# Optimization experiments

Measured on AMD Instinct MI355X. Metric: run time of the kernel, lower is better.

## Reference

```python
import jax, jax.numpy as jnp
import numpy as np
import math

B, S, K, D, H, LH, W, L = 8, 2048, 128, 512, 8, 4, 128, 4
DH = D // H           # 64, head dim
NW = S // W           # 16 windows
NUM_STEPS = 1000
RESCALE = 4000.0


def setup_inputs() -> dict:
    key = jax.random.key(0)
    ks = iter(jax.random.split(key, 48))
    def rn(shape, s=0.02):
        return jax.random.normal(next(ks), shape, dtype=jnp.float32) * s
    return {
        "x": jax.random.normal(next(ks), (B, S, K), dtype=jnp.float32),
        "t": jax.random.randint(next(ks), (B,), 0, NUM_STEPS, dtype=jnp.int32),
        "token_w": rn((K, D)), "token_b": jnp.zeros((D,), jnp.float32),
        "ax1": rn((NW, D), 1.0), "ax2": rn((W, D), 1.0),
        "time_w1": rn((D, 4 * D)), "time_b1": jnp.zeros((4 * D,), jnp.float32),
        "time_w2": rn((4 * D, D)), "time_b2": jnp.zeros((D,), jnp.float32),
        "ln1_g": jnp.ones((L, D), jnp.float32), "ln1_b": jnp.zeros((L, D), jnp.float32),
        "wq": rn((L, D, D)), "wk": rn((L, D, D)), "wv": rn((L, D, D)),
        "wo": rn((L, D, D)), "wo_b": jnp.zeros((L, D), jnp.float32),
        "ln2_g": jnp.ones((L, D), jnp.float32), "ln2_b": jnp.zeros((L, D), jnp.float32),
        "ff_w1": rn((L, D, 4 * D)), "ff_b1": jnp.zeros((L, 4 * D), jnp.float32),
        "ff_w2": rn((L, 4 * D, D)), "ff_b2": jnp.zeros((L, D), jnp.float32),
        "norm_g": jnp.ones((D,), jnp.float32), "norm_b": jnp.zeros((D,), jnp.float32),
        "out_w": rn((D, K)), "out_b": jnp.zeros((K,), jnp.float32),
        "alpha": jax.random.normal(next(ks), (1,), dtype=jnp.float32),
    }


def _layernorm(x, g, b, eps=1e-5):
    mu = x.mean(-1, keepdims=True)
    var = ((x - mu) ** 2).mean(-1, keepdims=True)
    return (x - mu) * jax.lax.rsqrt(var + eps) * g + b


def _mish(x):
    return x * jnp.tanh(jax.nn.softplus(x))


def _sinusoidal(t):
    # SinusoidalPosEmb(dim=D, num_steps=NUM_STEPS, rescale_steps=4000)
    tt = t.astype(jnp.float32) / NUM_STEPS * RESCALE
    half = D // 2
    freqs = jnp.exp(jnp.arange(half, dtype=jnp.float32) * (-math.log(10000.0) / (half - 1)))
    e = tt[:, None] * freqs[None, :]
    return jnp.concatenate([jnp.sin(e), jnp.cos(e)], axis=-1)  # (B, D)


def _linear_attn(q, k, v):
    # non-causal kernelized linear attention; q,k,v: (B, h, S, dh)
    scale = DH ** -0.25
    q = jax.nn.softmax(q * scale, axis=-1)   # softmax over feature dim
    k = jax.nn.softmax(k * scale, axis=-2)   # softmax over sequence dim
    ctx = jnp.einsum('bhnd,bhne->bhde', k, v)
    return jnp.einsum('bhnd,bhde->bhne', q, ctx)


def _local_attn(q, k, v):
    # windowed softmax attention, window W, look_backward=1, look_forward=1
    b, h = q.shape[0], q.shape[1]
    qw = q.reshape(b, h, NW, W, DH) * (DH ** -0.5)
    def look_around(x):
        xw = x.reshape(b, h, NW, W, DH)
        xp = jnp.pad(xw, ((0, 0), (0, 0), (1, 1), (0, 0), (0, 0)))
        # keys of windows [i-1, i, i+1] -> (b, h, NW, 3W, dh)
        return jnp.concatenate([xp[:, :, :-2], xp[:, :, 1:-1], xp[:, :, 2:]], axis=3)
    kw, vw = look_around(k), look_around(v)
    win = jnp.arange(NW)[:, None] + (jnp.arange(3 * W) // W)[None, :] - 1  # (NW, 3W)
    valid = (win >= 0) & (win < NW)
    dots = jnp.einsum('bhnwd,bhnkd->bhnwk', qw, kw)
    mask_value = -jnp.finfo(dots.dtype).max
    dots = jnp.where(valid[None, None, :, None, :], dots, mask_value)
    attn = jax.nn.softmax(dots, axis=-1)
    out = jnp.einsum('bhnwk,bhnkd->bhnwd', attn, vw)
    return out.reshape(b, h, S, DH)


def reference(x, t, token_w, token_b, ax1, ax2, time_w1, time_b1, time_w2, time_b2,
              ln1_g, ln1_b, wq, wk, wv, wo, wo_b, ln2_g, ln2_b,
              ff_w1, ff_b1, ff_w2, ff_b2, norm_g, norm_b, out_w, out_b, alpha):
    te = _sinusoidal(t)
    te = _mish(te @ time_w1 + time_b1) @ time_w2 + time_b2          # (B, D)
    h = x @ token_w + token_b                                        # token embedding
    pos = (ax1[:, None, :] + ax2[None, :, :]).reshape(S, D)          # axial pos emb (summed)
    h = h + pos[None] + te[:, None, :]
    for l in range(L):
        n = _layernorm(h, ln1_g[l], ln1_b[l])
        def split_heads(y):
            return y.reshape(B, S, H, DH).transpose(0, 2, 1, 3)
        q = split_heads(n @ wq[l]); k = split_heads(n @ wk[l]); v = split_heads(n @ wv[l])
        lo = _local_attn(q[:, :LH], k[:, :LH], v[:, :LH])            # local heads first
        gl = _linear_attn(q[:, LH:], k[:, LH:], v[:, LH:])           # global linear-attn heads
        a = jnp.concatenate([lo, gl], axis=1).transpose(0, 2, 1, 3).reshape(B, S, D)
        h = h + a @ wo[l] + wo_b[l]
        n = _layernorm(h, ln2_g[l], ln2_b[l])
        h = h + jax.nn.gelu(n @ ff_w1[l] + ff_b1[l], approximate=False) @ ff_w2[l] + ff_b2[l]
    out = _layernorm(h, norm_g, norm_b) @ out_w + out_b              # (B, S, K)
    return alpha * out.transpose(0, 2, 1)                            # permute + Rezero -> (B, K, S)
```

## Files before the change

### kernel.cpp

```cpp
#include <hip/hip_runtime.h>

typedef __bf16 bf16;
typedef float f32x4 __attribute__((ext_vector_type(4)));
typedef __bf16 b8v __attribute__((ext_vector_type(8)));
typedef __bf16 b4v __attribute__((ext_vector_type(4)));

#define S_LEN 2048
#define DMODEL 512
#define KDIM 128
#define NWIN 16
#define WIN 128
#define QKVS 1536

__device__ inline f32x4 mfma16(b8v a, b8v b, f32x4 c) {
  return __builtin_amdgcn_mfma_f32_16x16x32_bf16(a, b, c, 0, 0, 0);
}

__device__ inline void gload16(const bf16* g, bf16* l) {
  __builtin_amdgcn_global_load_lds(
      (const __attribute__((address_space(1))) void*)g,
      (__attribute__((address_space(3))) void*)l, 16, 0, 0);
}

template<int N>
__device__ inline void waitvm() { asm volatile("s_waitcnt vmcnt(%0)" :: "n"(N) : "memory"); }
template<int N>
__device__ inline void waitlgkm() { asm volatile("s_waitcnt lgkmcnt(%0)" :: "n"(N) : "memory"); }
__device__ inline void barrier_raw() { asm volatile("s_barrier" ::: "memory"); }


__global__ __launch_bounds__(256) void conv_kernel(const float* __restrict__ in, bf16* __restrict__ out, int n) {
  int i4 = (blockIdx.x * 256 + threadIdx.x) * 4;
  if (i4 < n) {
    float4 v = *(const float4*)(in + i4);
    b4v o; o[0] = (bf16)v.x; o[1] = (bf16)v.y; o[2] = (bf16)v.z; o[3] = (bf16)v.w;
    *(b4v*)(out + i4) = o;
  }
}

__global__ __launch_bounds__(256) void convT_kernel(const float* __restrict__ W, bf16* __restrict__ WT,
                                                    int Kd, int N, size_t in_ls, size_t out_ls) {
  __shared__ float tile[32][33];
  int k0 = blockIdx.x * 32, n0 = blockIdx.y * 32;
  const float* Wl = W + (size_t)blockIdx.z * in_ls;
  bf16* WTl = WT + (size_t)blockIdx.z * out_ls;
  int tx = threadIdx.x & 31, ty = threadIdx.x >> 5;
  #pragma unroll
  for (int i = 0; i < 4; i++)
    tile[ty + i*8][tx] = Wl[(size_t)(k0 + ty + i*8) * N + n0 + tx];
  __syncthreads();
  #pragma unroll
  for (int i = 0; i < 4; i++)
    WTl[(size_t)(n0 + ty + i*8) * Kd + k0 + tx] = (bf16)tile[tx][ty + i*8];
}

__global__ __launch_bounds__(256) void convT4_kernel(
    const float* __restrict__ wq, const float* __restrict__ wk,
    const float* __restrict__ wv, const float* __restrict__ wo,
    bf16* __restrict__ wqkvT, bf16* __restrict__ woT) {
  __shared__ float tile[32][33];
  int z = blockIdx.z, layer = z >> 2, which = z & 3;
  const float* W = (which == 0 ? wq : which == 1 ? wk : which == 2 ? wv : wo)
                   + (size_t)layer * 262144;
  bf16* WT = (which < 3) ? (wqkvT + (size_t)layer * 786432 + (size_t)which * 262144)
                         : (woT + (size_t)layer * 262144);
  int k0 = blockIdx.x * 32, n0 = blockIdx.y * 32;
  int tx = threadIdx.x & 31, ty = threadIdx.x >> 5;
  #pragma unroll
  for (int i = 0; i < 4; i++)
    tile[ty + i*8][tx] = W[(size_t)(k0 + ty + i*8) * 512 + n0 + tx];
  __syncthreads();
  #pragma unroll
  for (int i = 0; i < 4; i++)
    WT[(size_t)(n0 + ty + i*8) * 512 + k0 + tx] = (bf16)tile[tx][ty + i*8];
}


__global__ __launch_bounds__(256) void time1_kernel(const int* __restrict__ t,
    const float* __restrict__ w1, const float* __restrict__ b1, float* __restrict__ te1) {
  __shared__ float te[512];
  __shared__ float red[4][64];
  int b = blockIdx.x >> 5;
  int c0 = (blockIdx.x & 31) * 64;
  int tid = threadIdx.x;
  float tt = (float)t[b] * 4.0f;
  {
    float fr = expf((float)tid * (-9.210340371976184f / 255.0f));
    float e = tt * fr;
    te[tid] = sinf(e);
    te[tid + 256] = cosf(e);
  }
  __syncthreads();
  int lane = tid & 63, wv = tid >> 6;
  float acc = 0.f;
  const float* wcol = w1 + (size_t)(wv * 128) * 2048 + c0 + lane;
  for (int dd = 0; dd < 128; dd++) acc = fmaf(te[wv * 128 + dd], wcol[(size_t)dd * 2048], acc);
  red[wv][lane] = acc;
  __syncthreads();
  if (tid < 64) {
    float a = red[0][tid] + red[1][tid] + red[2][tid] + red[3][tid] + b1[c0 + tid];
    float sp = (a > 20.f) ? a : log1pf(expf(a));
    te1[b * 2048 + c0 + tid] = a * tanhf(sp);
  }
}

__global__ __launch_bounds__(256) void time2_kernel(const float* __restrict__ te1,
    const float* __restrict__ w2, const float* __restrict__ b2, float* __restrict__ te2) {
  __shared__ float hb[2048];
  __shared__ float red[4][64];
  int b = blockIdx.x >> 3;
  int c0 = (blockIdx.x & 7) * 64;
  int tid = threadIdx.x;
  for (int i = tid; i < 2048; i += 256) hb[i] = te1[b * 2048 + i];
  __syncthreads();
  int lane = tid & 63, wv = tid >> 6;
  float acc = 0.f;
  const float* wcol = w2 + (size_t)(wv * 512) * 512 + c0 + lane;
  for (int dd = 0; dd < 512; dd++) acc = fmaf(hb[wv * 512 + dd], wcol[(size_t)dd * 512], acc);
  red[wv][lane] = acc;
  __syncthreads();
  if (tid < 64)
    te2[b * 512 + c0 + tid] = red[0][tid] + red[1][tid] + red[2][tid] + red[3][tid] + b2[c0 + tid];
}


__global__ __launch_bounds__(256) void ln_kernel(const bf16* __restrict__ hsrc,
    const float* __restrict__ gg, const float* __restrict__ bb, bf16* __restrict__ out) {
  int row = blockIdx.x * 4 + (threadIdx.x >> 6);
  int lane = threadIdx.x & 63;
  const bf16* hr = hsrc + (size_t)row * 512 + lane * 8;
  b8v hv = *(const b8v*)hr;
  float xv[8];
  #pragma unroll
  for (int j = 0; j < 8; j++) xv[j] = (float)hv[j];
  float s = 0.f;
  #pragma unroll
  for (int j = 0; j < 8; j++) s += xv[j];
  #pragma unroll
  for (int off = 1; off < 64; off <<= 1) s += __shfl_xor(s, off);
  float mu = s * (1.f / 512.f);
  float vs = 0.f;
  #pragma unroll
  for (int j = 0; j < 8; j++) { float dd = xv[j] - mu; vs += dd * dd; }
  #pragma unroll
  for (int off = 1; off < 64; off <<= 1) vs += __shfl_xor(vs, off);
  float rstd = 1.f / sqrtf(vs * (1.f / 512.f) + 1e-5f);
  int dbase = lane * 8;
  bf16* orow = out + (size_t)row * 512 + dbase;
  #pragma unroll
  for (int j = 0; j < 8; j++)
    orow[j] = (bf16)((xv[j] - mu) * rstd * gg[dbase + j] + bb[dbase + j]);
}

template<int EPI, int BM, int BN>
__global__ __launch_bounds__(512, 2) void gemm3_kernel(
    const bf16* __restrict__ A, const bf16* __restrict__ BT,
    const float* __restrict__ bias, bf16* __restrict__ Cb,
    int N, int Kd, int nbx) {
  constexpr int LA = BM / 128;
  constexpr int LB = BN / 128;
  constexpr int LPI = LA + LB;
  constexpr int EA = BM * 32;
  constexpr int EB = BN * 32;
  constexpr int ER = EA + EB;
  constexpr int MF = BM / 32;
  constexpr int NF = BN / 64;
  __shared__ bf16 lds[ER * 3];
  int tid = threadIdx.x;
  int lane = tid & 63, wid = tid >> 6;
  int g = lane >> 4, lr = lane & 15;
  int wm = wid >> 2, wn = wid & 3;
  int p = blockIdx.x;
  int cpx = (int)gridDim.x >> 3;
  int vid = (p & 7) * cpx + (p >> 3);
  int m0 = (vid / nbx) * BM;
  int n0 = (vid % nbx) * BN;
  f32x4 acc[MF][NF] = {};
  int rl = tid >> 2;
  int csw = ((tid & 3) ^ ((rl >> 1) & 3)) * 8;
  const bf16* pa = A + (size_t)(m0 + rl) * Kd + csw;
  const bf16* pb = BT + (size_t)(n0 + rl) * Kd + csw;
  int NT = Kd >> 5;
  auto stage = [&](int t, int buf) {
    int k0 = t << 5;
    bf16* base = lds + buf * ER + (wid << 9);
    #pragma unroll
    for (int rr = 0; rr < LA; rr++)
      gload16(pa + (size_t)(rr * 128) * Kd + k0, base + rr * 4096);
    #pragma unroll
    for (int rr = 0; rr < LB; rr++)
      gload16(pb + (size_t)(rr * 128) * Kd + k0, base + EA + rr * 4096);
  };
  stage(0, 0);
  stage(1, 1);
  for (int kt = 0; kt < NT; ++kt) {
    if (kt + 1 < NT) waitvm<LPI>();
    else             waitvm<0>();
    barrier_raw();
    const bf16* ba = lds + (kt % 3) * ER;
    const bf16* bb = ba + EA;
    if (kt + 2 < NT) stage(kt + 2, (kt + 2) % 3);
    b8v af[MF], bfr[NF];
    #pragma unroll
    for (int i = 0; i < MF; i++) {
      int ra = wm * (BM / 2) + i * 16 + lr;
      af[i] = *(const b8v*)(ba + ra * 32 + ((g * 8) ^ (((ra >> 1) & 3) << 3)));
    }
    #pragma unroll
    for (int j0 = 0; j0 < 2; j0++) {
      int rb = wn * (BN / 4) + j0 * 16 + lr;
      bfr[j0] = *(const b8v*)(bb + rb * 32 + ((g * 8) ^ (((rb >> 1) & 3) << 3)));
    }
    waitlgkm<0>();
    __builtin_amdgcn_sched_barrier(0);
    __builtin_amdgcn_s_setprio(1);
    #pragma unroll
    for (int i = 0; i < MF; i++) acc[i][0] = mfma16(af[i], bfr[0], acc[i][0]);
    __builtin_amdgcn_s_setprio(0);
    #pragma unroll
    for (int j = 1; j < NF; j++) {
      if (j + 1 < NF) {
        int rb = wn * (BN / 4) + (j + 1) * 16 + lr;
        bfr[j + 1] = *(const b8v*)(bb + rb * 32 + ((g * 8) ^ (((rb >> 1) & 3) << 3)));
        waitlgkm<1>();
      } else {
        waitlgkm<0>();
      }
      __builtin_amdgcn_sched_barrier(0);
      __builtin_amdgcn_s_setprio(1);
      #pragma unroll
      for (int i = 0; i < MF; i++) acc[i][j] = mfma16(af[i], bfr[j], acc[i][j]);
      __builtin_amdgcn_s_setprio(0);
    }
  }
  #pragma unroll
  for (int i = 0; i < MF; i++) {
    #pragma unroll
    for (int j = 0; j < NF; j++) {
      int col = n0 + wn * (BN / 4) + j * 16 + lr;
      float bv = (EPI != 0) ? bias[col] : 0.0f;
      #pragma unroll
      for (int r = 0; r < 4; r++) {
        int row = m0 + wm * (BM / 2) + i * 16 + g * 4 + r;
        float v = acc[i][j][r] + bv;
        if (EPI == 0) {
          Cb[(size_t)row * N + col] = (bf16)v;
        } else if (EPI == 2) {
          size_t idx = (size_t)row * N + col;
          Cb[idx] = (bf16)((float)Cb[idx] + v);
        } else if (EPI == 3) {
          float u = 1.5957691216057308f * (v + 0.044715f * v * v * v);
          float ge = v / (1.0f + __expf(-u));
          Cb[(size_t)row * N + col] = (bf16)ge;
        }
      }
    }
  }
}

template<int EPI>
__global__ __launch_bounds__(256) void gemm_kernel(
    const bf16* __restrict__ A, const bf16* __restrict__ BT,
    const float* __restrict__ bias, float* __restrict__ Cf, bf16* __restrict__ Cb,
    int N, int Kd, int nbx,
    const float* __restrict__ q1, const float* __restrict__ q2, const float* __restrict__ q3,
    const float* __restrict__ alphap) {
  __shared__ bf16 As[2][4096];
  __shared__ bf16 Bs[2][4096];
  int tid = threadIdx.x;
  int lane = tid & 63, wid = tid >> 6;
  int g = lane >> 4, lr = lane & 15;
  int wm = wid >> 1, wn = wid & 1;
  int p = blockIdx.x;
  int cpx = (int)gridDim.x >> 3;
  int vid = (p & 7) * cpx + (p >> 3);
  int m0 = (vid / nbx) * 128;
  int n0 = (vid % nbx) * 128;
  f32x4 acc[4][4] = {};
  int srow = wid * 16 + (lane >> 2);
  int scol = (lane & 3) * 8;
  const bf16* pa = A + (size_t)(m0 + srow) * Kd + scol;
  const bf16* pb = BT + (size_t)(n0 + srow) * Kd + scol;
  const size_t rstep = (size_t)64 * Kd;
  int nt = Kd >> 5;
  auto stage = [&](int buf, int k0) {
    bf16* lA = &As[buf][wid * 512];
    bf16* lB = &Bs[buf][wid * 512];
    gload16(pa + k0, lA);
    gload16(pa + rstep + k0, lA + 2048);
    gload16(pb + k0, lB);
    gload16(pb + rstep + k0, lB + 2048);
  };
  stage(0, 0);
  __syncthreads();
  int cur = 0;
  for (int t = 0; t < nt; ++t) {
    if (t + 1 < nt) stage(cur ^ 1, (t + 1) * 32);
    b8v af[4], bfv[4];
    #pragma unroll
    for (int i = 0; i < 4; i++) af[i]  = *(const b8v*)&As[cur][(wm * 64 + i * 16 + lr) * 32 + g * 8];
    #pragma unroll
    for (int i = 0; i < 4; i++) bfv[i] = *(const b8v*)&Bs[cur][(wn * 64 + i * 16 + lr) * 32 + g * 8];
    #pragma unroll
    for (int mf = 0; mf < 4; mf++)
      #pragma unroll
      for (int nf = 0; nf < 4; nf++)
        acc[mf][nf] = mfma16(af[mf], bfv[nf], acc[mf][nf]);
    __syncthreads();
    cur ^= 1;
  }
  if constexpr (EPI == 4) {
    __shared__ float Ts[32][130];
    float alp = alphap[0];
    int b_ = m0 >> 11, sb = m0 & 2047;
    #pragma unroll
    for (int cg = 0; cg < 4; cg++) {
      __syncthreads();
      if (wn == (cg >> 1)) {
        #pragma unroll
        for (int nfi = 0; nfi < 2; nfi++) {
          int nf = (cg & 1) * 2 + nfi;
          int cl = nfi * 16 + lr;
          float bv = bias[cg * 32 + cl];
          #pragma unroll
          for (int mf = 0; mf < 4; mf++)
            #pragma unroll
            for (int r = 0; r < 4; r++)
              Ts[cl][wm * 64 + mf * 16 + g * 4 + r] = alp * (acc[mf][nf][r] + bv);
        }
      }
      __syncthreads();
      int cl = tid >> 3, soff = (tid & 7) * 16;
      int col = cg * 32 + cl;
      float* dst = Cf + (size_t)b_ * (KDIM * S_LEN) + (size_t)col * S_LEN + sb + soff;
      #pragma unroll
      for (int q4 = 0; q4 < 4; q4++) {
        float4 v = {Ts[cl][soff + q4*4], Ts[cl][soff + q4*4 + 1], Ts[cl][soff + q4*4 + 2], Ts[cl][soff + q4*4 + 3]};
        *(float4*)(dst + q4 * 4) = v;
      }
    }
    return;
  }
  #pragma unroll
  for (int mf = 0; mf < 4; mf++) {
    #pragma unroll
    for (int nf = 0; nf < 4; nf++) {
      int col = n0 + wn * 64 + nf * 16 + lr;
      float bv = bias[col];
      #pragma unroll
      for (int r = 0; r < 4; r++) {
        int row = m0 + wm * 64 + mf * 16 + g * 4 + r;
        float v = acc[mf][nf][r] + bv;
        if (EPI == 5) {
          int b_ = row >> 11, s_ = row & 2047;
          float pv = q1[(s_ >> 7) * 512 + col] + q2[(s_ & 127) * 512 + col] + q3[b_ * 512 + col];
          Cb[(size_t)row * N + col] = (bf16)(v + pv);
        }
      }
    }
  }
}

__global__ __launch_bounds__(256) void locattn_kernel(
    const bf16* __restrict__ qkv, bf16* __restrict__ ab) {
  __shared__ bf16 Ks[128][72];
  __shared__ bf16 Vt[64][136];
  __shared__ bf16 Ps[4][32][136];
  int w = blockIdx.x;
  int b = blockIdx.y >> 2, hh = blockIdx.y & 3;
  int tid = threadIdx.x, wid = tid >> 6, lane = tid & 63;
  int g = lane >> 4, lr = lane & 15;
  const size_t rowb = (size_t)b * S_LEN * QKVS;
  int qrow0 = w * WIN + wid * 32;
  b8v qf[2][2];
  #pragma unroll
  for (int mf = 0; mf < 2; mf++)
    #pragma unroll
    for (int kf = 0; kf < 2; kf++)
      qf[mf][kf] = *(const b8v*)(qkv + rowb + (size_t)(qrow0 + mf * 16 + lr) * QKVS + hh * 64 + kf * 32 + g * 8);
  float mrun[2][4], lrun[2][4];
  f32x4 oacc[2][4] = {};
  #pragma unroll
  for (int mf = 0; mf < 2; mf++)
    #pragma unroll
    for (int r = 0; r < 4; r++) { mrun[mf][r] = -3e38f; lrun[mf][r] = 0.f; }
  for (int c = 0; c < 3; c++) {
    int wc = w - 1 + c;
    if (wc < 0 || wc >= NWIN) continue;
    __syncthreads();
    {
      int row = tid >> 1, f0 = (tid & 1) * 32;
      const bf16* kp = qkv + rowb + (size_t)(wc * WIN + row) * QKVS + 512 + hh * 64 + f0;
      #pragma unroll
      for (int i = 0; i < 4; i++)
        *(b8v*)&Ks[row][f0 + i * 8] = *(const b8v*)(kp + i * 8);
      const bf16* vp = qkv + rowb + (size_t)(wc * WIN + row) * QKVS + 1024 + hh * 64 + f0;
      #pragma unroll
      for (int i = 0; i < 4; i++) {
        b8v vv = *(const b8v*)(vp + i * 8);
        #pragma unroll
        for (int j = 0; j < 8; j++) Vt[f0 + i * 8 + j][row] = vv[j];
      }
    }
    __syncthreads();
    f32x4 sc[2][8] = {};
    #pragma unroll
    for (int nf = 0; nf < 8; nf++) {
      #pragma unroll
      for (int kf = 0; kf < 2; kf++) {
        b8v kfr = *(const b8v*)&Ks[nf * 16 + lr][kf * 32 + g * 8];
        sc[0][nf] = mfma16(qf[0][kf], kfr, sc[0][nf]);
        sc[1][nf] = mfma16(qf[1][kf], kfr, sc[1][nf]);
      }
    }
    #pragma unroll
    for (int mf = 0; mf < 2; mf++) {
      #pragma unroll
      for (int r = 0; r < 4; r++) {
        float cm = -3e38f;
        #pragma unroll
        for (int nf = 0; nf < 8; nf++) { sc[mf][nf][r] *= 0.125f; cm = fmaxf(cm, sc[mf][nf][r]); }
        cm = fmaxf(cm, __shfl_xor(cm, 1));
        cm = fmaxf(cm, __shfl_xor(cm, 2));
        cm = fmaxf(cm, __shfl_xor(cm, 4));
        cm = fmaxf(cm, __shfl_xor(cm, 8));
        float mnew = fmaxf(mrun[mf][r], cm);
        float corr = __expf(mrun[mf][r] - mnew);
        float rs = 0.f;
        #pragma unroll
        for (int nf = 0; nf < 8; nf++) { float p = __expf(sc[mf][nf][r] - mnew); sc[mf][nf][r] = p; rs += p; }
        rs += __shfl_xor(rs, 1); rs += __shfl_xor(rs, 2);
        rs += __shfl_xor(rs, 4); rs += __shfl_xor(rs, 8);
        lrun[mf][r] = lrun[mf][r] * corr + rs;
        mrun[mf][r] = mnew;
        #pragma unroll
        for (int vf = 0; vf < 4; vf++) oacc[mf][vf][r] *= corr;
      }
    }
    #pragma unroll
    for (int mf = 0; mf < 2; mf++)
      #pragma unroll
      for (int nf = 0; nf < 8; nf++)
        #pragma unroll
        for (int r = 0; r < 4; r++)
          Ps[wid][mf * 16 + g * 4 + r][nf * 16 + lr] = (bf16)sc[mf][nf][r];
    #pragma unroll
    for (int kf2 = 0; kf2 < 4; kf2++) {
      b8v pa0 = *(const b8v*)&Ps[wid][lr][kf2 * 32 + g * 8];
      b8v pa1 = *(const b8v*)&Ps[wid][16 + lr][kf2 * 32 + g * 8];
      #pragma unroll
      for (int vf = 0; vf < 4; vf++) {
        b8v vv = *(const b8v*)&Vt[vf * 16 + lr][kf2 * 32 + g * 8];
        oacc[0][vf] = mfma16(pa0, vv, oacc[0][vf]);
        oacc[1][vf] = mfma16(pa1, vv, oacc[1][vf]);
      }
    }
  }
  #pragma unroll
  for (int mf = 0; mf < 2; mf++) {
    #pragma unroll
    for (int r = 0; r < 4; r++) {
      float inv = 1.0f / lrun[mf][r];
      int row = qrow0 + mf * 16 + g * 4 + r;
      #pragma unroll
      for (int vf = 0; vf < 4; vf++)
        ab[(size_t)b * S_LEN * DMODEL + (size_t)row * DMODEL + hh * 64 + vf * 16 + lr] = (bf16)(oacc[mf][vf][r] * inv);
    }
  }
}


__global__ __launch_bounds__(256) void la2_kernel(const bf16* __restrict__ qkv,
    float* __restrict__ part, float* __restrict__ psum) {
  int ch = blockIdx.x, bh = blockIdx.y;
  int b = bh >> 2, hh = bh & 3;
  __shared__ float ke[128][65];
  __shared__ float vsh[128][65];
  __shared__ float red[4][64];
  int tid = threadIdx.x;
  const float scale = 0.35355339059327373f;
  const size_t base = ((size_t)b * S_LEN + (size_t)ch * 128) * QKVS;
  const bf16* kp = qkv + base + 768 + hh * 64;
  const bf16* vp = qkv + base + 1280 + hh * 64;
  for (int i = tid; i < 1024; i += 256) {
    int s = i >> 3, d0 = (i & 7) * 8;
    b8v kv = *(const b8v*)(kp + (size_t)s * QKVS + d0);
    b8v vv = *(const b8v*)(vp + (size_t)s * QKVS + d0);
    #pragma unroll
    for (int j = 0; j < 8; j++) {
      ke[s][d0 + j] = __expf((float)kv[j] * scale);
      vsh[s][d0 + j] = (float)vv[j];
    }
  }
  __syncthreads();
  int d = tid & 63, sg = tid >> 6;
  float ps = 0.f;
  for (int s = sg * 32; s < sg * 32 + 32; s++) ps += ke[s][d];
  red[sg][d] = ps;
  int e = tid & 63, dg = tid >> 6;
  float accv[16] = {};
  for (int s = 0; s < 128; s++) {
    float vv2 = vsh[s][e];
    #pragma unroll
    for (int i = 0; i < 16; i++) accv[i] = fmaf(ke[s][dg * 16 + i], vv2, accv[i]);
  }
  __syncthreads();
  float* pp = part + ((size_t)ch * 32 + bh) * 4096 + (size_t)dg * 16 * 64 + e;
  #pragma unroll
  for (int i = 0; i < 16; i++) pp[i * 64] = accv[i];
  if (tid < 64)
    psum[((size_t)ch * 32 + bh) * 64 + tid] = red[0][tid] + red[1][tid] + red[2][tid] + red[3][tid];
}

__global__ __launch_bounds__(256) void la2b_kernel(const float* __restrict__ part,
    const float* __restrict__ psum, float* __restrict__ ctx) {
  int idx = blockIdx.x * 256 + threadIdx.x;
  int bh = idx >> 12;
  int d = (idx >> 6) & 63;
  float s = 0.f, cs = 0.f;
  for (int c = 0; c < 16; c++) {
    s += part[(size_t)c * 131072 + idx];
    cs += psum[(size_t)(c * 32 + bh) * 64 + d];
  }
  ctx[idx] = s / cs;
}

__global__ __launch_bounds__(256) void la3_kernel(const bf16* __restrict__ qkv,
    const float* __restrict__ ctx, bf16* __restrict__ ab) {
  int ch = blockIdx.x, bh = blockIdx.y;
  int b = bh >> 2, hh = bh & 3;
  __shared__ float cs[64][65];
  int tid = threadIdx.x;
  for (int i = tid; i < 4096; i += 256) cs[i >> 6][i & 63] = ctx[(size_t)bh * 4096 + i];
  __syncthreads();
  int s = ch * 128 + (tid >> 1);
  int e0 = (tid & 1) * 32;
  const float scale = 0.35355339059327373f;
  const bf16* qr = qkv + ((size_t)b * S_LEN + s) * QKVS + 256 + hh * 64;
  float qv[64];
  float mx = -3e38f;
  #pragma unroll
  for (int i = 0; i < 8; i++) {
    b8v qq = *(const b8v*)(qr + i * 8);
    #pragma unroll
    for (int j = 0; j < 8; j++) { qv[i * 8 + j] = (float)qq[j] * scale; mx = fmaxf(mx, qv[i * 8 + j]); }
  }
  float sum = 0.f;
  #pragma unroll
  for (int dd = 0; dd < 64; dd++) { qv[dd] = __expf(qv[dd] - mx); sum += qv[dd]; }
  float inv = 1.f / sum;
  float o[32] = {};
  #pragma unroll
  for (int dd = 0; dd < 64; dd++) {
    float qq = qv[dd] * inv;
    #pragma unroll
    for (int j = 0; j < 32; j++) o[j] = fmaf(qq, cs[dd][e0 + j], o[j]);
  }
  bf16* op = ab + ((size_t)b * S_LEN + s) * DMODEL + 256 + hh * 64 + e0;
  #pragma unroll
  for (int j = 0; j < 32; j++) op[j] = (bf16)o[j];
}


extern "C" void kernel_launch(void* const* d_in, const int* in_sizes, int n_in,
                              void* d_out, int out_size, void* d_ws, size_t ws_size,
                              hipStream_t stream) {
  (void)in_sizes; (void)n_in; (void)out_size; (void)ws_size;
  const float* x_f     = (const float*)d_in[0];
  const int*   t_i     = (const int*)  d_in[1];
  const float* token_w = (const float*)d_in[2];
  const float* token_b = (const float*)d_in[3];
  const float* ax1     = (const float*)d_in[4];
  const float* ax2     = (const float*)d_in[5];
  const float* time_w1 = (const float*)d_in[6];
  const float* time_b1 = (const float*)d_in[7];
  const float* time_w2 = (const float*)d_in[8];
  const float* time_b2 = (const float*)d_in[9];
  const float* ln1_g   = (const float*)d_in[10];
  const float* ln1_b   = (const float*)d_in[11];
  const float* wq      = (const float*)d_in[12];
  const float* wk      = (const float*)d_in[13];
  const float* wv      = (const float*)d_in[14];
  const float* wo      = (const float*)d_in[15];
  const float* wo_b    = (const float*)d_in[16];
  const float* ln2_g   = (const float*)d_in[17];
  const float* ln2_b   = (const float*)d_in[18];
  const float* ff_w1   = (const float*)d_in[19];
  const float* ff_b1   = (const float*)d_in[20];
  const float* ff_w2   = (const float*)d_in[21];
  const float* ff_b2   = (const float*)d_in[22];
  const float* norm_g  = (const float*)d_in[23];
  const float* norm_b  = (const float*)d_in[24];
  const float* out_w   = (const float*)d_in[25];
  const float* out_b   = (const float*)d_in[26];
  const float* alpha   = (const float*)d_in[27];

  char* ws = (char*)d_ws;
  bf16*  h      = (bf16*)(ws + 0);
  float* te1    = (float*)(ws + 16777216);
  float* te2    = (float*)(ws + 16842752);
  float* psum   = (float*)(ws + 16859136);
  float* ctx    = (float*)(ws + 16990208);
  float* part   = (float*)(ws + 17514496);
  bf16* nbuf    = (bf16*)(ws + 25903104);
  bf16* qkvb    = (bf16*)(ws + 42680320);
  bf16* abuf    = (bf16*)(ws + 93011968);
  bf16* gbuf    = qkvb;
  bf16* xw      = (bf16*)(ws + 109789184);
  bf16* token_wT= (bf16*)(ws + 113983488);
  bf16* wqkvT   = (bf16*)(ws + 114114560);
  bf16* woT     = (bf16*)(ws + 120406016);
  bf16* ff1T    = (bf16*)(ws + 122503168);
  bf16* ff2T    = (bf16*)(ws + 130891776);
  bf16* outwT   = (bf16*)(ws + 139280384);

  conv_kernel<<<2048, 256, 0, stream>>>(x_f, xw, 2097152);
  convT_kernel<<<dim3(4, 16, 1),  256, 0, stream>>>(token_w, token_wT, 128, 512, 65536, 65536);
  convT4_kernel<<<dim3(16, 16, 16), 256, 0, stream>>>(wq, wk, wv, wo, wqkvT, woT);
  convT_kernel<<<dim3(16, 64, 4), 256, 0, stream>>>(ff_w1, ff1T, 512, 2048, 1048576, 1048576);
  convT_kernel<<<dim3(64, 16, 4), 256, 0, stream>>>(ff_w2, ff2T, 2048, 512, 1048576, 1048576);
  convT_kernel<<<dim3(16, 4, 1),  256, 0, stream>>>(out_w, outwT, 512, 128, 65536, 65536);

  time1_kernel<<<256, 256, 0, stream>>>(t_i, time_w1, time_b1, te1);
  time2_kernel<<<64, 256, 0, stream>>>(te1, time_w2, time_b2, te2);

  gemm_kernel<5><<<512, 256, 0, stream>>>(xw, token_wT, token_b, nullptr, h, 512, 128, 4, ax1, ax2, te2, nullptr);

  for (int l = 0; l < 4; l++) {
    ln_kernel<<<4096, 256, 0, stream>>>(h, ln1_g + l * 512, ln1_b + l * 512, nbuf);
    gemm3_kernel<0, 128, 256><<<768, 512, 0, stream>>>(nbuf, wqkvT + (size_t)l * 786432, nullptr, qkvb, 1536, 512, 6);
    locattn_kernel<<<dim3(16, 32), 256, 0, stream>>>(qkvb, abuf);
    la2_kernel<<<dim3(16, 32), 256, 0, stream>>>(qkvb, part, psum);
    la2b_kernel<<<512, 256, 0, stream>>>(part, psum, ctx);
    la3_kernel<<<dim3(16, 32), 256, 0, stream>>>(qkvb, ctx, abuf);
    gemm3_kernel<2, 128, 256><<<256, 512, 0, stream>>>(abuf, woT + (size_t)l * 262144, wo_b + l * 512, h, 512, 512, 2);
    ln_kernel<<<4096, 256, 0, stream>>>(h, ln2_g + l * 512, ln2_b + l * 512, nbuf);
    gemm3_kernel<3, 256, 256><<<512, 512, 0, stream>>>(nbuf, ff1T + (size_t)l * 1048576, ff_b1 + l * 2048, gbuf, 2048, 512, 8);
    gemm3_kernel<2, 128, 256><<<256, 512, 0, stream>>>(gbuf, ff2T + (size_t)l * 1048576, ff_b2 + l * 512, h, 512, 2048, 2);
  }

  ln_kernel<<<4096, 256, 0, stream>>>(h, norm_g, norm_b, nbuf);
  gemm_kernel<4><<<128, 256, 0, stream>>>(nbuf, outwT, out_b, (float*)d_out, nullptr, 128, 512, 1, nullptr, nullptr, nullptr, alpha);
}
```

Before: 1.039 ms.

## Merge local and linear-attention KV passes into one launch, fold ctx reduce into la3

Combines the local-window attention kernel and the linear-attention KV-partial kernel into one launch that branches on blockIdx.y, sharing a single shared-memory buffer. The separate la2b reduction kernel is removed: la3 now sums the per-chunk partials and normalizers itself. The FF1 GEMM tile is also changed from 256 to 128 rows with twice as many blocks. The goal is fewer launches and better overlap of independent attention work, at the cost of larger shared memory per block (lower occupancy) and each la3 block redundantly re-reducing 16 partial chunks.

```diff
diff --git a/kernel.cpp b/kernel.cpp
--- a/kernel.cpp
+++ b/kernel.cpp
@@ -361,177 +361,177 @@
   }
 }
 
-__global__ __launch_bounds__(256) void locattn_kernel(
-    const bf16* __restrict__ qkv, bf16* __restrict__ ab) {
-  __shared__ bf16 Ks[128][72];
-  __shared__ bf16 Vt[64][136];
-  __shared__ bf16 Ps[4][32][136];
-  int w = blockIdx.x;
-  int b = blockIdx.y >> 2, hh = blockIdx.y & 3;
-  int tid = threadIdx.x, wid = tid >> 6, lane = tid & 63;
-  int g = lane >> 4, lr = lane & 15;
-  const size_t rowb = (size_t)b * S_LEN * QKVS;
-  int qrow0 = w * WIN + wid * 32;
-  b8v qf[2][2];
-  #pragma unroll
-  for (int mf = 0; mf < 2; mf++)
-    #pragma unroll
-    for (int kf = 0; kf < 2; kf++)
-      qf[mf][kf] = *(const b8v*)(qkv + rowb + (size_t)(qrow0 + mf * 16 + lr) * QKVS + hh * 64 + kf * 32 + g * 8);
-  float mrun[2][4], lrun[2][4];
-  f32x4 oacc[2][4] = {};
-  #pragma unroll
-  for (int mf = 0; mf < 2; mf++)
-    #pragma unroll
-    for (int r = 0; r < 4; r++) { mrun[mf][r] = -3e38f; lrun[mf][r] = 0.f; }
-  for (int c = 0; c < 3; c++) {
-    int wc = w - 1 + c;
-    if (wc < 0 || wc >= NWIN) continue;
+__global__ __launch_bounds__(256) void attn_kernel(
+    const bf16* __restrict__ qkv, bf16* __restrict__ ab,
+    float* __restrict__ part, float* __restrict__ psum) {
+  __shared__ __align__(16) char smem[70656];
+  int tid = threadIdx.x;
+  if (blockIdx.y < 32) {
+    bf16 (*Ks)[72]  = (bf16(*)[72])(smem);
+    bf16 (*Vt)[136] = (bf16(*)[136])(smem + 18432);
+    bf16 (*Ps)[32][136] = (bf16(*)[32][136])(smem + 35840);
+    int w = blockIdx.x;
+    int b = blockIdx.y >> 2, hh = blockIdx.y & 3;
+    int wid = tid >> 6, lane = tid & 63;
+    int g = lane >> 4, lr = lane & 15;
+    const size_t rowb = (size_t)b * S_LEN * QKVS;
+    int qrow0 = w * WIN + wid * 32;
+    b8v qf[2][2];
+    #pragma unroll
+    for (int mf = 0; mf < 2; mf++)
+      #pragma unroll
+      for (int kf = 0; kf < 2; kf++)
+        qf[mf][kf] = *(const b8v*)(qkv + rowb + (size_t)(qrow0 + mf * 16 + lr) * QKVS + hh * 64 + kf * 32 + g * 8);
+    float mrun[2][4], lrun[2][4];
+    f32x4 oacc[2][4] = {};
+    #pragma unroll
+    for (int mf = 0; mf < 2; mf++)
+      #pragma unroll
+      for (int r = 0; r < 4; r++) { mrun[mf][r] = -3e38f; lrun[mf][r] = 0.f; }
+    for (int c = 0; c < 3; c++) {
+      int wc = w - 1 + c;
+      if (wc < 0 || wc >= NWIN) continue;
+      __syncthreads();
+      {
+        int row = tid >> 1, f0 = (tid & 1) * 32;
+        const bf16* kp = qkv + rowb + (size_t)(wc * WIN + row) * QKVS + 512 + hh * 64 + f0;
+        #pragma unroll
+        for (int i = 0; i < 4; i++)
+          *(b8v*)&Ks[row][f0 + i * 8] = *(const b8v*)(kp + i * 8);
+        const bf16* vp = qkv + rowb + (size_t)(wc * WIN + row) * QKVS + 1024 + hh * 64 + f0;
+        #pragma unroll
+        for (int i = 0; i < 4; i++) {
+          b8v vv = *(const b8v*)(vp + i * 8);
+          #pragma unroll
+          for (int j = 0; j < 8; j++) Vt[f0 + i * 8 + j][row] = vv[j];
+        }
+      }
+      __syncthreads();
+      f32x4 sc[2][8] = {};
+      #pragma unroll
+      for (int nf = 0; nf < 8; nf++) {
+        #pragma unroll
+        for (int kf = 0; kf < 2; kf++) {
+          b8v kfr = *(const b8v*)&Ks[nf * 16 + lr][kf * 32 + g * 8];
+          sc[0][nf] = mfma16(qf[0][kf], kfr, sc[0][nf]);
+          sc[1][nf] = mfma16(qf[1][kf], kfr, sc[1][nf]);
+        }
+      }
+      #pragma unroll
+      for (int mf = 0; mf < 2; mf++) {
+        #pragma unroll
+        for (int r = 0; r < 4; r++) {
+          float cm = -3e38f;
+          #pragma unroll
+          for (int nf = 0; nf < 8; nf++) { sc[mf][nf][r] *= 0.125f; cm = fmaxf(cm, sc[mf][nf][r]); }
+          cm = fmaxf(cm, __shfl_xor(cm, 1));
+          cm = fmaxf(cm, __shfl_xor(cm, 2));
+          cm = fmaxf(cm, __shfl_xor(cm, 4));
+          cm = fmaxf(cm, __shfl_xor(cm, 8));
+          float mnew = fmaxf(mrun[mf][r], cm);
+          float corr = __expf(mrun[mf][r] - mnew);
+          float rs = 0.f;
+          #pragma unroll
+          for (int nf = 0; nf < 8; nf++) { float pv = __expf(sc[mf][nf][r] - mnew); sc[mf][nf][r] = pv; rs += pv; }
+          rs += __shfl_xor(rs, 1); rs += __shfl_xor(rs, 2);
+          rs += __shfl_xor(rs, 4); rs += __shfl_xor(rs, 8);
+          lrun[mf][r] = lrun[mf][r] * corr + rs;
+          mrun[mf][r] = mnew;
+          #pragma unroll
+          for (int vf = 0; vf < 4; vf++) oacc[mf][vf][r] *= corr;
+        }
+      }
+      #pragma unroll
+      for (int mf = 0; mf < 2; mf++)
+        #pragma unroll
+        for (int nf = 0; nf < 8; nf++)
+          #pragma unroll
+          for (int r = 0; r < 4; r++)
+            Ps[wid][mf * 16 + g * 4 + r][nf * 16 + lr] = (bf16)sc[mf][nf][r];
+      #pragma unroll
+      for (int kf2 = 0; kf2 < 4; kf2++) {
+        b8v pa0 = *(const b8v*)&Ps[wid][lr][kf2 * 32 + g * 8];
+        b8v pa1 = *(const b8v*)&Ps[wid][16 + lr][kf2 * 32 + g * 8];
+        #pragma unroll
+        for (int vf = 0; vf < 4; vf++) {
+          b8v vv = *(const b8v*)&Vt[vf * 16 + lr][kf2 * 32 + g * 8];
+          oacc[0][vf] = mfma16(pa0, vv, oacc[0][vf]);
+          oacc[1][vf] = mfma16(pa1, vv, oacc[1][vf]);
+        }
+      }
+    }
+    #pragma unroll
+    for (int mf = 0; mf < 2; mf++) {
+      #pragma unroll
+      for (int r = 0; r < 4; r++) {
+        float inv = 1.0f / lrun[mf][r];
+        int row = qrow0 + mf * 16 + g * 4 + r;
+        #pragma unroll
+        for (int vf = 0; vf < 4; vf++)
+          ab[(size_t)b * S_LEN * DMODEL + (size_t)row * DMODEL + hh * 64 + vf * 16 + lr] = (bf16)(oacc[mf][vf][r] * inv);
+      }
+    }
+  } else {
+    float (*ke)[65]  = (float(*)[65])(smem);
+    float (*vsh)[65] = (float(*)[65])(smem + 33280);
+    float (*red)[64] = (float(*)[64])(smem + 66560);
+    int ch = blockIdx.x, bh = blockIdx.y - 32;
+    int b = bh >> 2, hh = bh & 3;
+    const float scale = 0.35355339059327373f;
+    const size_t base = ((size_t)b * S_LEN + (size_t)ch * 128) * QKVS;
+    const bf16* kp = qkv + base + 768 + hh * 64;
+    const bf16* vp = qkv + base + 1280 + hh * 64;
+    for (int i = tid; i < 1024; i += 256) {
+      int s = i >> 3, d0 = (i & 7) * 8;
+      b8v kv = *(const b8v*)(kp + (size_t)s * QKVS + d0);
+      b8v vv = *(const b8v*)(vp + (size_t)s * QKVS + d0);
+      #pragma unroll
+      for (int j = 0; j < 8; j++) {
+        ke[s][d0 + j] = __expf((float)kv[j] * scale);
+        vsh[s][d0 + j] = (float)vv[j];
+      }
+    }
     __syncthreads();
-    {
-      int row = tid >> 1, f0 = (tid & 1) * 32;
-      const bf16* kp = qkv + rowb + (size_t)(wc * WIN + row) * QKVS + 512 + hh * 64 + f0;
-      #pragma unroll
-      for (int i = 0; i < 4; i++)
-        *(b8v*)&Ks[row][f0 + i * 8] = *(const b8v*)(kp + i * 8);
-      const bf16* vp = qkv + rowb + (size_t)(wc * WIN + row) * QKVS + 1024 + hh * 64 + f0;
-      #pragma unroll
-      for (int i = 0; i < 4; i++) {
-        b8v vv = *(const b8v*)(vp + i * 8);
-        #pragma unroll
-        for (int j = 0; j < 8; j++) Vt[f0 + i * 8 + j][row] = vv[j];
-      }
+    int d = tid & 63, sg = tid >> 6;
+    float ps = 0.f;
+    for (int s = sg * 32; s < sg * 32 + 32; s++) ps += ke[s][d];
+    red[sg][d] = ps;
+    int e = tid & 63, dg = tid >> 6;
+    float accv[16] = {};
+    for (int s = 0; s < 128; s++) {
+      float vv2 = vsh[s][e];
+      #pragma unroll
+      for (int i = 0; i < 16; i++) accv[i] = fmaf(ke[s][dg * 16 + i], vv2, accv[i]);
     }
     __syncthreads();
-    f32x4 sc[2][8] = {};
-    #pragma unroll
-    for (int nf = 0; nf < 8; nf++) {
-      #pragma unroll
-      for (int kf = 0; kf < 2; kf++) {
-        b8v kfr = *(const b8v*)&Ks[nf * 16 + lr][kf * 32 + g * 8];
-        sc[0][nf] = mfma16(qf[0][kf], kfr, sc[0][nf]);
-        sc[1][nf] = mfma16(qf[1][kf], kfr, sc[1][nf]);
-      }
-    }
-    #pragma unroll
-    for (int mf = 0; mf < 2; mf++) {
-      #pragma unroll
-      for (int r = 0; r < 4; r++) {
-        float cm = -3e38f;
-        #pragma unroll
-        for (int nf = 0; nf < 8; nf++) { sc[mf][nf][r] *= 0.125f; cm = fmaxf(cm, sc[mf][nf][r]); }
-        cm = fmaxf(cm, __shfl_xor(cm, 1));
-        cm = fmaxf(cm, __shfl_xor(cm, 2));
-        cm = fmaxf(cm, __shfl_xor(cm, 4));
-        cm = fmaxf(cm, __shfl_xor(cm, 8));
-        float mnew = fmaxf(mrun[mf][r], cm);
-        float corr = __expf(mrun[mf][r] - mnew);
-        float rs = 0.f;
-        #pragma unroll
-        for (int nf = 0; nf < 8; nf++) { float p = __expf(sc[mf][nf][r] - mnew); sc[mf][nf][r] = p; rs += p; }
-        rs += __shfl_xor(rs, 1); rs += __shfl_xor(rs, 2);
-        rs += __shfl_xor(rs, 4); rs += __shfl_xor(rs, 8);
-        lrun[mf][r] = lrun[mf][r] * corr + rs;
-        mrun[mf][r] = mnew;
-        #pragma unroll
-        for (int vf = 0; vf < 4; vf++) oacc[mf][vf][r] *= corr;
-      }
-    }
-    #pragma unroll
-    for (int mf = 0; mf < 2; mf++)
-      #pragma unroll
-      for (int nf = 0; nf < 8; nf++)
-        #pragma unroll
-        for (int r = 0; r < 4; r++)
-          Ps[wid][mf * 16 + g * 4 + r][nf * 16 + lr] = (bf16)sc[mf][nf][r];
-    #pragma unroll
-    for (int kf2 = 0; kf2 < 4; kf2++) {
-      b8v pa0 = *(const b8v*)&Ps[wid][lr][kf2 * 32 + g * 8];
-      b8v pa1 = *(const b8v*)&Ps[wid][16 + lr][kf2 * 32 + g * 8];
-      #pragma unroll
-      for (int vf = 0; vf < 4; vf++) {
-        b8v vv = *(const b8v*)&Vt[vf * 16 + lr][kf2 * 32 + g * 8];
-        oacc[0][vf] = mfma16(pa0, vv, oacc[0][vf]);
-        oacc[1][vf] = mfma16(pa1, vv, oacc[1][vf]);
-      }
-    }
-  }
-  #pragma unroll
-  for (int mf = 0; mf < 2; mf++) {
-    #pragma unroll
-    for (int r = 0; r < 4; r++) {
-      float inv = 1.0f / lrun[mf][r];
-      int row = qrow0 + mf * 16 + g * 4 + r;
-      #pragma unroll
-      for (int vf = 0; vf < 4; vf++)
-        ab[(size_t)b * S_LEN * DMODEL + (size_t)row * DMODEL + hh * 64 + vf * 16 + lr] = (bf16)(oacc[mf][vf][r] * inv);
-    }
-  }
-}
-
-
-__global__ __launch_bounds__(256) void la2_kernel(const bf16* __restrict__ qkv,
-    float* __restrict__ part, float* __restrict__ psum) {
-  int ch = blockIdx.x, bh = blockIdx.y;
-  int b = bh >> 2, hh = bh & 3;
-  __shared__ float ke[128][65];
-  __shared__ float vsh[128][65];
-  __shared__ float red[4][64];
-  int tid = threadIdx.x;
-  const float scale = 0.35355339059327373f;
-  const size_t base = ((size_t)b * S_LEN + (size_t)ch * 128) * QKVS;
-  const bf16* kp = qkv + base + 768 + hh * 64;
-  const bf16* vp = qkv + base + 1280 + hh * 64;
-  for (int i = tid; i < 1024; i += 256) {
-    int s = i >> 3, d0 = (i & 7) * 8;
-    b8v kv = *(const b8v*)(kp + (size_t)s * QKVS + d0);
-    b8v vv = *(const b8v*)(vp + (size_t)s * QKVS + d0);
-    #pragma unroll
-    for (int j = 0; j < 8; j++) {
-      ke[s][d0 + j] = __expf((float)kv[j] * scale);
-      vsh[s][d0 + j] = (float)vv[j];
-    }
-  }
-  __syncthreads();
-  int d = tid & 63, sg = tid >> 6;
-  float ps = 0.f;
-  for (int s = sg * 32; s < sg * 32 + 32; s++) ps += ke[s][d];
-  red[sg][d] = ps;
-  int e = tid & 63, dg = tid >> 6;
-  float accv[16] = {};
-  for (int s = 0; s < 128; s++) {
-    float vv2 = vsh[s][e];
-    #pragma unroll
-    for (int i = 0; i < 16; i++) accv[i] = fmaf(ke[s][dg * 16 + i], vv2, accv[i]);
-  }
-  __syncthreads();
-  float* pp = part + ((size_t)ch * 32 + bh) * 4096 + (size_t)dg * 16 * 64 + e;
-  #pragma unroll
-  for (int i = 0; i < 16; i++) pp[i * 64] = accv[i];
-  if (tid < 64)
-    psum[((size_t)ch * 32 + bh) * 64 + tid] = red[0][tid] + red[1][tid] + red[2][tid] + red[3][tid];
-}
-
-__global__ __launch_bounds__(256) void la2b_kernel(const float* __restrict__ part,
-    const float* __restrict__ psum, float* __restrict__ ctx) {
-  int idx = blockIdx.x * 256 + threadIdx.x;
-  int bh = idx >> 12;
-  int d = (idx >> 6) & 63;
-  float s = 0.f, cs = 0.f;
-  for (int c = 0; c < 16; c++) {
-    s += part[(size_t)c * 131072 + idx];
-    cs += psum[(size_t)(c * 32 + bh) * 64 + d];
-  }
-  ctx[idx] = s / cs;
+    float* pp = part + ((size_t)ch * 32 + bh) * 4096 + (size_t)dg * 16 * 64 + e;
+    #pragma unroll
+    for (int i = 0; i < 16; i++) pp[i * 64] = accv[i];
+    if (tid < 64)
+      psum[((size_t)ch * 32 + bh) * 64 + tid] = red[0][tid] + red[1][tid] + red[2][tid] + red[3][tid];
+  }
 }
 
 __global__ __launch_bounds__(256) void la3_kernel(const bf16* __restrict__ qkv,
-    const float* __restrict__ ctx, bf16* __restrict__ ab) {
+    const float* __restrict__ part, const float* __restrict__ psum, bf16* __restrict__ ab) {
   int ch = blockIdx.x, bh = blockIdx.y;
   int b = bh >> 2, hh = bh & 3;
   __shared__ float cs[64][65];
+  __shared__ float csum[64];
   int tid = threadIdx.x;
-  for (int i = tid; i < 4096; i += 256) cs[i >> 6][i & 63] = ctx[(size_t)bh * 4096 + i];
+  if (tid < 64) {
+    float s = 0.f;
+    #pragma unroll
+    for (int c = 0; c < 16; c++) s += psum[(size_t)((c * 32 + bh) << 6) + tid];
+    csum[tid] = s;
+  }
+  __syncthreads();
+  for (int i = tid; i < 4096; i += 256) {
+    float s = 0.f;
+    #pragma unroll
+    for (int c = 0; c < 16; c++) s += part[((size_t)(c * 32 + bh) << 12) + i];
+    cs[i >> 6][i & 63] = s / csum[i >> 6];
+  }
   __syncthreads();
   int s = ch * 128 + (tid >> 1);
   int e0 = (tid & 1) * 32;
@@ -600,7 +600,6 @@
   float* te1    = (float*)(ws + 16777216);
   float* te2    = (float*)(ws + 16842752);
   float* psum   = (float*)(ws + 16859136);
-  float* ctx    = (float*)(ws + 16990208);
   float* part   = (float*)(ws + 17514496);
   bf16* nbuf    = (bf16*)(ws + 25903104);
   bf16* qkvb    = (bf16*)(ws + 42680320);
@@ -629,13 +628,11 @@
   for (int l = 0; l < 4; l++) {
     ln_kernel<<<4096, 256, 0, stream>>>(h, ln1_g + l * 512, ln1_b + l * 512, nbuf);
     gemm3_kernel<0, 128, 256><<<768, 512, 0, stream>>>(nbuf, wqkvT + (size_t)l * 786432, nullptr, qkvb, 1536, 512, 6);
-    locattn_kernel<<<dim3(16, 32), 256, 0, stream>>>(qkvb, abuf);
-    la2_kernel<<<dim3(16, 32), 256, 0, stream>>>(qkvb, part, psum);
-    la2b_kernel<<<512, 256, 0, stream>>>(part, psum, ctx);
-    la3_kernel<<<dim3(16, 32), 256, 0, stream>>>(qkvb, ctx, abuf);
+    attn_kernel<<<dim3(16, 64), 256, 0, stream>>>(qkvb, abuf, part, psum);
+    la3_kernel<<<dim3(16, 32), 256, 0, stream>>>(qkvb, part, psum, abuf);
     gemm3_kernel<2, 128, 256><<<256, 512, 0, stream>>>(abuf, woT + (size_t)l * 262144, wo_b + l * 512, h, 512, 512, 2);
     ln_kernel<<<4096, 256, 0, stream>>>(h, ln2_g + l * 512, ln2_b + l * 512, nbuf);
-    gemm3_kernel<3, 256, 256><<<512, 512, 0, stream>>>(nbuf, ff1T + (size_t)l * 1048576, ff_b1 + l * 2048, gbuf, 2048, 512, 8);
+    gemm3_kernel<3, 128, 256><<<1024, 512, 0, stream>>>(nbuf, ff1T + (size_t)l * 1048576, ff_b1 + l * 2048, gbuf, 2048, 512, 8);
     gemm3_kernel<2, 128, 256><<<256, 512, 0, stream>>>(gbuf, ff2T + (size_t)l * 1048576, ff_b2 + l * 512, h, 512, 2048, 2);
   }
 
```

Measured after the change: 1.042 ms. Within noise of the previous version (+0.2%).
